# Performance work log

Hardware: AMD Instinct MI355X
Metric: run time of the kernel (lower is better)

Reference implementation:

```python
import jax, jax.numpy as jnp
import numpy as np

HEADS = 16
DIM_HEAD = 64
SCALE = DIM_HEAD ** -0.5
LN_EPS = 1e-5


def setup_inputs() -> dict:
    key = jax.random.key(0)
    ks = jax.random.split(key, 4)
    B, N, D = 2, 2048, 1024
    inner = HEADS * DIM_HEAD  # 1024
    x = jax.random.normal(ks[0], (B, N, D), dtype=jnp.float32)
    m = jax.random.normal(ks[1], (B, N, N), dtype=jnp.float32)
    gamma = jnp.ones((D,), dtype=jnp.float32)
    beta = jnp.zeros((D,), dtype=jnp.float32)
    W_qkv = jax.random.normal(ks[2], (D, 3 * inner), dtype=jnp.float32) * (D ** -0.5)
    W_out = jax.random.normal(ks[3], (inner, D), dtype=jnp.float32) * (inner ** -0.5)
    return {"x": x, "m": m, "gamma": gamma, "beta": beta, "W_qkv": W_qkv, "W_out": W_out}


def reference(x, m, gamma, beta, W_qkv, W_out):
    B, N, D = x.shape
    # LayerNorm
    mu = jnp.mean(x, axis=-1, keepdims=True)
    var = jnp.var(x, axis=-1, keepdims=True)
    xn = (x - mu) * jax.lax.rsqrt(var + LN_EPS) * gamma + beta
    # QKV projection (no bias)
    qkv = xn @ W_qkv  # [B, N, 3*inner]
    q, k, v = jnp.split(qkv, 3, axis=-1)
    split_heads = lambda t: t.reshape(B, N, HEADS, DIM_HEAD).transpose(0, 2, 1, 3)  # b h n d
    q, k, v = split_heads(q), split_heads(k), split_heads(v)
    # Non-standard order: mask added BEFORE scaling
    qk = jnp.einsum('bhid,bhjd->bhij', q, k)
    dots = (qk + m[:, None, :, :]) * SCALE
    attn = jax.nn.softmax(dots, axis=-1)
    out = jnp.einsum('bhij,bhjd->bhid', attn, v)
    out = out.transpose(0, 2, 1, 3).reshape(B, N, HEADS * DIM_HEAD)
    return out @ W_out  # dropout is identity at inference
```

## Files before the change

kernel.cpp:

```cpp
#include <hip/hip_runtime.h>
#include <hip/hip_bf16.h>
#include <math.h>

typedef _Float16 f16;
typedef _Float16 f16x4 __attribute__((ext_vector_type(4)));
typedef _Float16 f16x8 __attribute__((ext_vector_type(8)));
typedef float f32x4 __attribute__((ext_vector_type(4)));

#define HD 64
#define NH 16
#define BATCH 2
#define SEQ 2048
#define DMODEL 1024
#define NQKV 3072
#define ROWS 4096
#define NEG_BIG (-1.0e30f)
#define SCALE_LOG2E 0.18033688011112042f

__device__ __forceinline__ f32x4 mfma16h(f16x8 a, f16x8 b, f32x4 c){
  return __builtin_amdgcn_mfma_f32_16x16x32_f16(a, b, c, 0, 0, 0);
}

__device__ __forceinline__ void gload16(const f16* g, f16* l){
  __builtin_amdgcn_global_load_lds(
      (const __attribute__((address_space(1))) unsigned int*)(g),
      (__attribute__((address_space(3))) unsigned int*)(l), 16, 0, 0);
}

__global__ __launch_bounds__(256) void ln_kernel(const float* __restrict__ x,
    const float* __restrict__ gamma, const float* __restrict__ beta,
    f16* __restrict__ xn)
{
  int row = blockIdx.x;
  int tid = threadIdx.x;
  float4 v = ((const float4*)(x + (size_t)row * DMODEL))[tid];
  float s  = v.x + v.y + v.z + v.w;
  float s2 = v.x*v.x + v.y*v.y + v.z*v.z + v.w*v.w;
  #pragma unroll
  for (int off = 32; off; off >>= 1){ s += __shfl_xor(s, off); s2 += __shfl_xor(s2, off); }
  __shared__ float red[8];
  int wave = tid >> 6, lane = tid & 63;
  if (lane == 0){ red[wave] = s; red[4 + wave] = s2; }
  __syncthreads();
  s  = red[0] + red[1] + red[2] + red[3];
  s2 = red[4] + red[5] + red[6] + red[7];
  float mu  = s * (1.f / DMODEL);
  float var = s2 * (1.f / DMODEL) - mu * mu;
  float rs  = rsqrtf(var + 1e-5f);
  float4 g  = ((const float4*)gamma)[tid];
  float4 be = ((const float4*)beta)[tid];
  f16x4 o;
  o[0] = (f16)((v.x - mu) * rs * g.x + be.x);
  o[1] = (f16)((v.y - mu) * rs * g.y + be.y);
  o[2] = (f16)((v.z - mu) * rs * g.z + be.z);
  o[3] = (f16)((v.w - mu) * rs * g.w + be.w);
  *(f16x4*)(xn + (size_t)row * DMODEL + tid*4) = o;
}

__global__ __launch_bounds__(256) void transpose_f2h_kernel(const float* __restrict__ in,
    f16* __restrict__ out, int R, int C)
{
  __shared__ float t[32][33];
  int c0 = blockIdx.x * 32, r0 = blockIdx.y * 32;
  int lx = threadIdx.x & 31, ly = threadIdx.x >> 5;
  #pragma unroll
  for (int i = 0; i < 32; i += 8) t[ly + i][lx] = in[(size_t)(r0 + ly + i) * C + c0 + lx];
  __syncthreads();
  #pragma unroll
  for (int i = 0; i < 32; i += 8) out[(size_t)(c0 + ly + i) * R + r0 + lx] = (f16)t[lx][ly + i];
}


__global__ __launch_bounds__(256, 3) void gemm_qkv(const f16* __restrict__ A,
    const f16* __restrict__ Bt, f16* __restrict__ Qo, f16* __restrict__ Ko,
    f16* __restrict__ Vo)
{
  __shared__ __align__(16) f16 As[2][128][32];
  __shared__ __align__(16) f16 Bs[2][128][32];
  const int K = DMODEL;
  int bm = blockIdx.y * 128, bn = blockIdx.x * 128;
  int tid = threadIdx.x;
  int wave = tid >> 6, lane = tid & 63, quad = lane >> 4, l15 = lane & 15;
  int mw = (wave >> 1) * 64, nw = (wave & 1) * 64;

  int sr0 = wave*16 + (lane >> 2);
  int sr1 = sr0 + 64;
  int sc  = (lane & 3) ^ (sr0 & 3);
  const f16* Ag = A  + (size_t)bm * K;
  const f16* Bg = Bt + (size_t)bn * K;
  f16* ldsA0 = &As[0][wave*16     ][0];
  f16* ldsA1 = &As[0][wave*16 + 64][0];
  f16* ldsB0 = &Bs[0][wave*16     ][0];
  f16* ldsB1 = &Bs[0][wave*16 + 64][0];

#define QSTAGE(buf, k0) do{ \
    gload16(Ag + (size_t)sr0 * K + (k0) + sc*8, ldsA0 + (buf)*4096); \
    gload16(Ag + (size_t)sr1 * K + (k0) + sc*8, ldsA1 + (buf)*4096); \
    gload16(Bg + (size_t)sr0 * K + (k0) + sc*8, ldsB0 + (buf)*4096); \
    gload16(Bg + (size_t)sr1 * K + (k0) + sc*8, ldsB1 + (buf)*4096); }while(0)

  f32x4 zero = {0.f, 0.f, 0.f, 0.f};
  f32x4 acc[4][4];
  #pragma unroll
  for (int i = 0; i < 4; i++)
    #pragma unroll
    for (int j = 0; j < 4; j++) acc[i][j] = zero;

  QSTAGE(0, 0);
  const int NS = K / 32;
  for (int it = 0; it < NS; ++it){
    int cur = it & 1;
    asm volatile("s_waitcnt vmcnt(0)" ::: "memory");
    __syncthreads();
    if (it + 1 < NS) QSTAGE(cur ^ 1, (it + 1) * 32);
    int ca = (quad ^ (l15 & 3)) * 8;
    f16x8 af[4], bfr[4];
    #pragma unroll
    for (int i = 0; i < 4; i++) af[i]  = *(const f16x8*)&As[cur][mw + i*16 + l15][ca];
    #pragma unroll
    for (int i = 0; i < 4; i++) bfr[i] = *(const f16x8*)&Bs[cur][nw + i*16 + l15][ca];
    __builtin_amdgcn_s_setprio(1);
    #pragma unroll
    for (int mi = 0; mi < 4; mi++)
      #pragma unroll
      for (int ni = 0; ni < 4; ni++)
        acc[mi][ni] = mfma16h(af[mi], bfr[ni], acc[mi][ni]);
    __builtin_amdgcn_s_setprio(0);
  }
#undef QSTAGE

  #pragma unroll
  for (int mi = 0; mi < 4; mi++){
    #pragma unroll
    for (int ni = 0; ni < 4; ni++){
      #pragma unroll
      for (int reg = 0; reg < 4; reg++){
        int r = bm + mw + mi*16 + quad*4 + reg;
        int c = bn + nw + ni*16 + l15;
        float v = acc[mi][ni][reg];
        int which = c >> 10;
        int hc = c & 1023;
        int h = hc >> 6, d = hc & 63;
        int b = r >> 11, nseq = r & 2047;
        size_t bh = (size_t)(b * NH + h);
        if (which == 0)      Qo[(bh * SEQ + nseq) * HD + d] = (f16)v;
        else if (which == 1) Ko[(bh * SEQ + nseq) * HD + d] = (f16)v;
        else                 Vo[(bh * HD + d) * SEQ + nseq] = (f16)v;
      }
    }
  }
}

__global__ __launch_bounds__(256, 3) void gemm_out(const f16* __restrict__ A,
    const f16* __restrict__ Bt, float* __restrict__ C, int M, int N, int K)
{
  __shared__ __align__(16) f16 As[2][128][32];
  __shared__ __align__(16) f16 Bs[2][128][32];
  int bm = blockIdx.y * 128, bn = blockIdx.x * 128;
  int tid = threadIdx.x;
  int wave = tid >> 6, lane = tid & 63, quad = lane >> 4, l15 = lane & 15;
  int mw = (wave >> 1) * 64, nw = (wave & 1) * 64;

  int sr0 = wave*16 + (lane >> 2);
  int sr1 = sr0 + 64;
  int sc  = (lane & 3) ^ (sr0 & 3);
  const f16* Ag = A  + (size_t)bm * K;
  const f16* Bg = Bt + (size_t)bn * K;
  f16* ldsA0 = &As[0][wave*16     ][0];
  f16* ldsA1 = &As[0][wave*16 + 64][0];
  f16* ldsB0 = &Bs[0][wave*16     ][0];
  f16* ldsB1 = &Bs[0][wave*16 + 64][0];

#define OSTAGE(buf, k0) do{ \
    gload16(Ag + (size_t)sr0 * K + (k0) + sc*8, ldsA0 + (buf)*4096); \
    gload16(Ag + (size_t)sr1 * K + (k0) + sc*8, ldsA1 + (buf)*4096); \
    gload16(Bg + (size_t)sr0 * K + (k0) + sc*8, ldsB0 + (buf)*4096); \
    gload16(Bg + (size_t)sr1 * K + (k0) + sc*8, ldsB1 + (buf)*4096); }while(0)

  f32x4 zero = {0.f, 0.f, 0.f, 0.f};
  f32x4 acc[4][4];
  #pragma unroll
  for (int i = 0; i < 4; i++)
    #pragma unroll
    for (int j = 0; j < 4; j++) acc[i][j] = zero;

  OSTAGE(0, 0);
  const int NS = 1024 / 32;
  for (int it = 0; it < NS; ++it){
    int cur = it & 1;
    asm volatile("s_waitcnt vmcnt(0)" ::: "memory");
    __syncthreads();
    if (it + 1 < NS) OSTAGE(cur ^ 1, (it + 1) * 32);
    int ca = (quad ^ (l15 & 3)) * 8;
    f16x8 af[4], bfr[4];
    #pragma unroll
    for (int i = 0; i < 4; i++) af[i]  = *(const f16x8*)&As[cur][mw + i*16 + l15][ca];
    #pragma unroll
    for (int i = 0; i < 4; i++) bfr[i] = *(const f16x8*)&Bs[cur][nw + i*16 + l15][ca];
    __builtin_amdgcn_s_setprio(1);
    #pragma unroll
    for (int mi = 0; mi < 4; mi++)
      #pragma unroll
      for (int ni = 0; ni < 4; ni++)
        acc[mi][ni] = mfma16h(af[mi], bfr[ni], acc[mi][ni]);
    __builtin_amdgcn_s_setprio(0);
  }
#undef OSTAGE

  #pragma unroll
  for (int mi = 0; mi < 4; mi++)
    #pragma unroll
    for (int ni = 0; ni < 4; ni++)
      #pragma unroll
      for (int reg = 0; reg < 4; reg++){
        int r = bm + mw + mi*16 + quad*4 + reg;
        int c = bn + nw + ni*16 + l15;
        C[(size_t)r * N + c] = acc[mi][ni][reg];
      }
}

__global__ __launch_bounds__(256, 4) void attn_kernel(const f16* __restrict__ Q,
    const f16* __restrict__ Kb, const f16* __restrict__ Vt,
    const float* __restrict__ mask, f16* __restrict__ Ao)
{
  __shared__ __align__(16) f16 KsB[2][64*64];
  __shared__ __align__(16) f16 VsB[2][64*64];
  __shared__ __align__(16) f16 Ps[4*16*64];

  int bh = blockIdx.y; int b = bh >> 4; int h = bh & 15;
  int q0 = blockIdx.x * 64;
  int tid = threadIdx.x;
  int wave = tid >> 6, lane = tid & 63, quad = lane >> 4, l15 = lane & 15;

  int rA = (wave*2 + 0)*8 + (lane >> 3);
  int rB = (wave*2 + 1)*8 + (lane >> 3);
  int cp = lane & 7;
  int ccA = cp ^ (rA & 7);
  int ccB = cp ^ (rB & 7);
  const f16* Kg = Kb + (size_t)bh * SEQ * HD;
  const f16* Vg = Vt + (size_t)bh * HD * SEQ;
  f16* ldsKA = &KsB[0][0] + (wave*2 + 0)*8*64;
  f16* ldsKB = &KsB[0][0] + (wave*2 + 1)*8*64;
  f16* ldsVA = &VsB[0][0] + (wave*2 + 0)*8*64;
  f16* ldsVB = &VsB[0][0] + (wave*2 + 1)*8*64;

  f16x8 qf[2];
  {
    const f16* qrow = Q + ((size_t)bh * SEQ + q0 + wave*16 + l15) * HD + quad*8;
    qf[0] = *(const f16x8*)(qrow);
    qf[1] = *(const f16x8*)(qrow + 32);
  }

  const float* mrow = mask + ((size_t)b * SEQ + q0 + wave*16 + l15) * SEQ + quad*4;

  gload16(Kg + (size_t)(0 + rA)*HD + ccA*8, ldsKA);
  gload16(Kg + (size_t)(0 + rB)*HD + ccB*8, ldsKB);
  gload16(Vg + (size_t)rA*SEQ + 0 + ccA*8, ldsVA);
  gload16(Vg + (size_t)rB*SEQ + 0 + ccB*8, ldsVB);

  f32x4 zero = {0.f, 0.f, 0.f, 0.f};
  f32x4 O[4];
  #pragma unroll
  for (int nt = 0; nt < 4; nt++) O[nt] = zero;
  float mrun = NEG_BIG, lrun = 0.f;

  const int NT = SEQ / 64;
  for (int it = 0; it < NT; ++it){
    int cur = it & 1;
    int j0 = it * 64;
    asm volatile("s_waitcnt vmcnt(0)" ::: "memory");
    __syncthreads();
    if (it + 1 < NT){
      int nb = cur ^ 1;
      int j0n = j0 + 64;
      gload16(Kg + (size_t)(j0n + rA)*HD + ccA*8, ldsKA + nb*4096);
      gload16(Kg + (size_t)(j0n + rB)*HD + ccB*8, ldsKB + nb*4096);
      gload16(Vg + (size_t)rA*SEQ + j0n + ccA*8, ldsVA + nb*4096);
      gload16(Vg + (size_t)rB*SEQ + j0n + ccB*8, ldsVB + nb*4096);
    }
    const f16* Ksc = &KsB[cur][0];
    const f16* Vsc = &VsB[cur][0];

    float sv[4][4];
    __builtin_amdgcn_s_setprio(1);
    #pragma unroll
    for (int jt = 0; jt < 4; jt++){
      f32x4 a = zero;
      int r = jt*16 + l15;
      #pragma unroll
      for (int kk = 0; kk < 2; kk++){
        f16x8 kf = *(const f16x8*)&Ksc[r*64 + (((kk*4 + quad) ^ (r & 7))*8)];
        a = mfma16h(kf, qf[kk], a);
      }
      float4 mv = *(const float4*)(mrow + j0 + jt*16);
      sv[jt][0] = (a[0] + mv.x) * SCALE_LOG2E;
      sv[jt][1] = (a[1] + mv.y) * SCALE_LOG2E;
      sv[jt][2] = (a[2] + mv.z) * SCALE_LOG2E;
      sv[jt][3] = (a[3] + mv.w) * SCALE_LOG2E;
    }
    __builtin_amdgcn_s_setprio(0);

    float m0 = fmaxf(fmaxf(sv[0][0], sv[0][1]), fmaxf(sv[0][2], sv[0][3]));
    float m1 = fmaxf(fmaxf(sv[1][0], sv[1][1]), fmaxf(sv[1][2], sv[1][3]));
    float m2 = fmaxf(fmaxf(sv[2][0], sv[2][1]), fmaxf(sv[2][2], sv[2][3]));
    float m3 = fmaxf(fmaxf(sv[3][0], sv[3][1]), fmaxf(sv[3][2], sv[3][3]));
    float tmax = fmaxf(fmaxf(m0, m1), fmaxf(m2, m3));
    tmax = fmaxf(tmax, __shfl_xor(tmax, 16));
    tmax = fmaxf(tmax, __shfl_xor(tmax, 32));

    if (__any(tmax > mrun + 8.f)){
      float nm = fmaxf(mrun, tmax);
      float alpha = exp2f(mrun - nm);
      mrun = nm;
      lrun *= alpha;
      float aR[4];
      #pragma unroll
      for (int reg = 0; reg < 4; reg++)
        aR[reg] = __shfl(alpha, (lane & 48) | (quad*4 + reg));
      #pragma unroll
      for (int nt = 0; nt < 4; nt++)
        #pragma unroll
        for (int reg = 0; reg < 4; reg++) O[nt][reg] *= aR[reg];
    }

    float ps = 0.f;
    #pragma unroll
    for (int jt = 0; jt < 4; jt++)
      #pragma unroll
      for (int reg = 0; reg < 4; reg++){
        float p = exp2f(sv[jt][reg] - mrun);
        sv[jt][reg] = p; ps += p;
      }
    ps += __shfl_xor(ps, 16);
    ps += __shfl_xor(ps, 32);
    lrun += ps;

    #pragma unroll
    for (int jt = 0; jt < 4; jt++){
      f16x4 ph;
      ph[0] = (f16)sv[jt][0]; ph[1] = (f16)sv[jt][1];
      ph[2] = (f16)sv[jt][2]; ph[3] = (f16)sv[jt][3];
      *(f16x4*)&Ps[wave*1024 + l15*64 + (((jt*2 + (quad>>1)) ^ (l15 & 7))*8) + (quad & 1)*4] = ph;
    }

    __builtin_amdgcn_s_setprio(1);
    #pragma unroll
    for (int nt = 0; nt < 4; nt++){
      #pragma unroll
      for (int kk = 0; kk < 2; kk++){
        int rv = nt*16 + l15;
        f16x8 pf = *(const f16x8*)&Ps[wave*1024 + l15*64 + (((kk*4 + quad) ^ (l15 & 7))*8)];
        f16x8 vf = *(const f16x8*)&Vsc[rv*64 + (((kk*4 + quad) ^ (rv & 7))*8)];
        O[nt] = mfma16h(pf, vf, O[nt]);
      }
    }
    __builtin_amdgcn_s_setprio(0);
  }

  float lR[4];
  #pragma unroll
  for (int reg = 0; reg < 4; reg++)
    lR[reg] = __shfl(lrun, (lane & 48) | (quad*4 + reg));
  #pragma unroll
  for (int nt = 0; nt < 4; nt++){
    #pragma unroll
    for (int reg = 0; reg < 4; reg++){
      float o = O[nt][reg] / lR[reg];
      int r = q0 + wave*16 + quad*4 + reg;
      Ao[((size_t)(b * SEQ + r)) * DMODEL + h * HD + nt*16 + l15] = (f16)o;
    }
  }
}

extern "C" void kernel_launch(void* const* d_in, const int* in_sizes, int n_in,
                              void* d_out, int out_size, void* d_ws, size_t ws_size,
                              hipStream_t stream)
{
  (void)in_sizes; (void)n_in; (void)out_size; (void)ws_size;
  const float* x     = (const float*)d_in[0];
  const float* m     = (const float*)d_in[1];
  const float* gamma = (const float*)d_in[2];
  const float* beta  = (const float*)d_in[3];
  const float* Wqkv  = (const float*)d_in[4];
  const float* Wout  = (const float*)d_in[5];
  float* out = (float*)d_out;

  char* ws = (char*)d_ws;
  f16* xn    = (f16*)(ws + 0);
  f16* Ao    = (f16*)(ws + 0);
  f16* Qb    = (f16*)(ws + 8388608);
  f16* WoutT = (f16*)(ws + 8388608);
  f16* Kbuf  = (f16*)(ws + 16777216);
  f16* Vtb   = (f16*)(ws + 25165824);
  f16* WqkvT = (f16*)(ws + 33554432);

  ln_kernel<<<ROWS, 256, 0, stream>>>(x, gamma, beta, xn);
  transpose_f2h_kernel<<<dim3(NQKV/32, DMODEL/32), 256, 0, stream>>>(Wqkv, WqkvT, DMODEL, NQKV);
  gemm_qkv<<<dim3(NQKV/128, ROWS/128), 256, 0, stream>>>(xn, WqkvT, Qb, Kbuf, Vtb);
  attn_kernel<<<dim3(SEQ/64, BATCH*NH), 256, 0, stream>>>(Qb, Kbuf, Vtb, m, Ao);
  transpose_f2h_kernel<<<dim3(DMODEL/32, DMODEL/32), 256, 0, stream>>>(Wout, WoutT, DMODEL, DMODEL);
  gemm_out<<<dim3(DMODEL/128, ROWS/128), 256, 0, stream>>>(Ao, WoutT, out, ROWS, DMODEL, DMODEL);
}
```

Before: 270.2 us.

## Load K/V fragments directly into registers in attention, halve gemm_out M tile

The attention kernel no longer stages K and V through double-buffered LDS with barriers. Each wave loads its K and V MFMA fragments straight from global memory into registers, prefetching the next K tile during the softmax. The per-tile cross-lane row-sum shuffle is deferred to a single reduction after the loop. The output GEMM tile is reduced from 128x128 to 64x128 to launch more blocks, at the cost of redundant per-wave global loads of K/V (no sharing across waves) and higher register pressure.

Result: slower. 450.1 us (+66.6%).

```diff
diff --git a/kernel.cpp b/kernel.cpp
--- a/kernel.cpp
+++ b/kernel.cpp
@@ -70,7 +70,6 @@
   for (int i = 0; i < 32; i += 8) out[(size_t)(c0 + ly + i) * R + r0 + lx] = (f16)t[lx][ly + i];
 }
 
-
 __global__ __launch_bounds__(256, 3) void gemm_qkv(const f16* __restrict__ A,
     const f16* __restrict__ Bt, f16* __restrict__ Qo, f16* __restrict__ Ko,
     f16* __restrict__ Vo)
@@ -151,55 +150,52 @@
   }
 }
 
-__global__ __launch_bounds__(256, 3) void gemm_out(const f16* __restrict__ A,
+__global__ __launch_bounds__(256, 4) void gemm_out(const f16* __restrict__ A,
     const f16* __restrict__ Bt, float* __restrict__ C, int M, int N, int K)
 {
-  __shared__ __align__(16) f16 As[2][128][32];
+  __shared__ __align__(16) f16 As[2][64][32];
   __shared__ __align__(16) f16 Bs[2][128][32];
-  int bm = blockIdx.y * 128, bn = blockIdx.x * 128;
+  int bm = blockIdx.y * 64, bn = blockIdx.x * 128;
   int tid = threadIdx.x;
   int wave = tid >> 6, lane = tid & 63, quad = lane >> 4, l15 = lane & 15;
-  int mw = (wave >> 1) * 64, nw = (wave & 1) * 64;
+  int mw = (wave >> 1) * 32, nw = (wave & 1) * 64;
 
   int sr0 = wave*16 + (lane >> 2);
-  int sr1 = sr0 + 64;
   int sc  = (lane & 3) ^ (sr0 & 3);
   const f16* Ag = A  + (size_t)bm * K;
   const f16* Bg = Bt + (size_t)bn * K;
   f16* ldsA0 = &As[0][wave*16     ][0];
-  f16* ldsA1 = &As[0][wave*16 + 64][0];
   f16* ldsB0 = &Bs[0][wave*16     ][0];
   f16* ldsB1 = &Bs[0][wave*16 + 64][0];
 
 #define OSTAGE(buf, k0) do{ \
-    gload16(Ag + (size_t)sr0 * K + (k0) + sc*8, ldsA0 + (buf)*4096); \
-    gload16(Ag + (size_t)sr1 * K + (k0) + sc*8, ldsA1 + (buf)*4096); \
+    gload16(Ag + (size_t)sr0 * K + (k0) + sc*8, ldsA0 + (buf)*2048); \
     gload16(Bg + (size_t)sr0 * K + (k0) + sc*8, ldsB0 + (buf)*4096); \
-    gload16(Bg + (size_t)sr1 * K + (k0) + sc*8, ldsB1 + (buf)*4096); }while(0)
+    gload16(Bg + (size_t)(sr0 + 64) * K + (k0) + sc*8, ldsB1 + (buf)*4096); }while(0)
 
   f32x4 zero = {0.f, 0.f, 0.f, 0.f};
-  f32x4 acc[4][4];
-  #pragma unroll
-  for (int i = 0; i < 4; i++)
+  f32x4 acc[2][4];
+  #pragma unroll
+  for (int i = 0; i < 2; i++)
     #pragma unroll
     for (int j = 0; j < 4; j++) acc[i][j] = zero;
 
   OSTAGE(0, 0);
-  const int NS = 1024 / 32;
+  const int NS = DMODEL / 32;
   for (int it = 0; it < NS; ++it){
     int cur = it & 1;
     asm volatile("s_waitcnt vmcnt(0)" ::: "memory");
     __syncthreads();
     if (it + 1 < NS) OSTAGE(cur ^ 1, (it + 1) * 32);
     int ca = (quad ^ (l15 & 3)) * 8;
-    f16x8 af[4], bfr[4];
-    #pragma unroll
-    for (int i = 0; i < 4; i++) af[i]  = *(const f16x8*)&As[cur][mw + i*16 + l15][ca];
+    f16x8 af[2], bfr[4];
+    #pragma unroll
+    for (int i = 0; i < 2; i++) af[i]  = *(const f16x8*)&As[cur][mw + i*16 + l15][ca];
     #pragma unroll
     for (int i = 0; i < 4; i++) bfr[i] = *(const f16x8*)&Bs[cur][nw + i*16 + l15][ca];
     __builtin_amdgcn_s_setprio(1);
     #pragma unroll
-    for (int mi = 0; mi < 4; mi++)
+    for (int mi = 0; mi < 2; mi++)
       #pragma unroll
       for (int ni = 0; ni < 4; ni++)
         acc[mi][ni] = mfma16h(af[mi], bfr[ni], acc[mi][ni]);
@@ -208,7 +204,7 @@
 #undef OSTAGE
 
   #pragma unroll
-  for (int mi = 0; mi < 4; mi++)
+  for (int mi = 0; mi < 2; mi++)
     #pragma unroll
     for (int ni = 0; ni < 4; ni++)
       #pragma unroll
@@ -219,12 +215,10 @@
       }
 }
 
-__global__ __launch_bounds__(256, 4) void attn_kernel(const f16* __restrict__ Q,
+__global__ __launch_bounds__(256, 3) void attn_kernel(const f16* __restrict__ Q,
     const f16* __restrict__ Kb, const f16* __restrict__ Vt,
     const float* __restrict__ mask, f16* __restrict__ Ao)
 {
-  __shared__ __align__(16) f16 KsB[2][64*64];
-  __shared__ __align__(16) f16 VsB[2][64*64];
   __shared__ __align__(16) f16 Ps[4*16*64];
 
   int bh = blockIdx.y; int b = bh >> 4; int h = bh & 15;
@@ -232,17 +226,8 @@
   int tid = threadIdx.x;
   int wave = tid >> 6, lane = tid & 63, quad = lane >> 4, l15 = lane & 15;
 
-  int rA = (wave*2 + 0)*8 + (lane >> 3);
-  int rB = (wave*2 + 1)*8 + (lane >> 3);
-  int cp = lane & 7;
-  int ccA = cp ^ (rA & 7);
-  int ccB = cp ^ (rB & 7);
   const f16* Kg = Kb + (size_t)bh * SEQ * HD;
   const f16* Vg = Vt + (size_t)bh * HD * SEQ;
-  f16* ldsKA = &KsB[0][0] + (wave*2 + 0)*8*64;
-  f16* ldsKB = &KsB[0][0] + (wave*2 + 1)*8*64;
-  f16* ldsVA = &VsB[0][0] + (wave*2 + 0)*8*64;
-  f16* ldsVB = &VsB[0][0] + (wave*2 + 1)*8*64;
 
   f16x8 qf[2];
   {
@@ -253,52 +238,55 @@
 
   const float* mrow = mask + ((size_t)b * SEQ + q0 + wave*16 + l15) * SEQ + quad*4;
 
-  gload16(Kg + (size_t)(0 + rA)*HD + ccA*8, ldsKA);
-  gload16(Kg + (size_t)(0 + rB)*HD + ccB*8, ldsKB);
-  gload16(Vg + (size_t)rA*SEQ + 0 + ccA*8, ldsVA);
-  gload16(Vg + (size_t)rB*SEQ + 0 + ccB*8, ldsVB);
-
   f32x4 zero = {0.f, 0.f, 0.f, 0.f};
   f32x4 O[4];
   #pragma unroll
   for (int nt = 0; nt < 4; nt++) O[nt] = zero;
   float mrun = NEG_BIG, lrun = 0.f;
 
+  f16x8 kf[8];
+  #pragma unroll
+  for (int jt = 0; jt < 4; jt++)
+    #pragma unroll
+    for (int kk = 0; kk < 2; kk++)
+      kf[jt*2+kk] = *(const f16x8*)(Kg + (size_t)(jt*16 + l15)*HD + kk*32 + quad*8);
+
   const int NT = SEQ / 64;
+  #pragma unroll 1
   for (int it = 0; it < NT; ++it){
-    int cur = it & 1;
     int j0 = it * 64;
-    asm volatile("s_waitcnt vmcnt(0)" ::: "memory");
-    __syncthreads();
-    if (it + 1 < NT){
-      int nb = cur ^ 1;
-      int j0n = j0 + 64;
-      gload16(Kg + (size_t)(j0n + rA)*HD + ccA*8, ldsKA + nb*4096);
-      gload16(Kg + (size_t)(j0n + rB)*HD + ccB*8, ldsKB + nb*4096);
-      gload16(Vg + (size_t)rA*SEQ + j0n + ccA*8, ldsVA + nb*4096);
-      gload16(Vg + (size_t)rB*SEQ + j0n + ccB*8, ldsVB + nb*4096);
-    }
-    const f16* Ksc = &KsB[cur][0];
-    const f16* Vsc = &VsB[cur][0];
+    int jn = (j0 + 64) & (SEQ - 1);
+
+    f16x8 vf[8];
+    #pragma unroll
+    for (int nt = 0; nt < 4; nt++)
+      #pragma unroll
+      for (int kk = 0; kk < 2; kk++)
+        vf[nt*2+kk] = *(const f16x8*)(Vg + (size_t)(nt*16 + l15)*SEQ + j0 + kk*32 + quad*8);
+
+    float4 mv[4];
+    #pragma unroll
+    for (int jt = 0; jt < 4; jt++) mv[jt] = *(const float4*)(mrow + j0 + jt*16);
 
     float sv[4][4];
     __builtin_amdgcn_s_setprio(1);
     #pragma unroll
     for (int jt = 0; jt < 4; jt++){
       f32x4 a = zero;
-      int r = jt*16 + l15;
-      #pragma unroll
-      for (int kk = 0; kk < 2; kk++){
-        f16x8 kf = *(const f16x8*)&Ksc[r*64 + (((kk*4 + quad) ^ (r & 7))*8)];
-        a = mfma16h(kf, qf[kk], a);
-      }
-      float4 mv = *(const float4*)(mrow + j0 + jt*16);
-      sv[jt][0] = (a[0] + mv.x) * SCALE_LOG2E;
-      sv[jt][1] = (a[1] + mv.y) * SCALE_LOG2E;
-      sv[jt][2] = (a[2] + mv.z) * SCALE_LOG2E;
-      sv[jt][3] = (a[3] + mv.w) * SCALE_LOG2E;
+      a = mfma16h(kf[jt*2 + 0], qf[0], a);
+      a = mfma16h(kf[jt*2 + 1], qf[1], a);
+      sv[jt][0] = (a[0] + mv[jt].x) * SCALE_LOG2E;
+      sv[jt][1] = (a[1] + mv[jt].y) * SCALE_LOG2E;
+      sv[jt][2] = (a[2] + mv[jt].z) * SCALE_LOG2E;
+      sv[jt][3] = (a[3] + mv[jt].w) * SCALE_LOG2E;
     }
     __builtin_amdgcn_s_setprio(0);
+
+    #pragma unroll
+    for (int jt = 0; jt < 4; jt++)
+      #pragma unroll
+      for (int kk = 0; kk < 2; kk++)
+        kf[jt*2+kk] = *(const f16x8*)(Kg + (size_t)(jn + jt*16 + l15)*HD + kk*32 + quad*8);
 
     float m0 = fmaxf(fmaxf(sv[0][0], sv[0][1]), fmaxf(sv[0][2], sv[0][3]));
     float m1 = fmaxf(fmaxf(sv[1][0], sv[1][1]), fmaxf(sv[1][2], sv[1][3]));
@@ -331,8 +319,6 @@
         float p = exp2f(sv[jt][reg] - mrun);
         sv[jt][reg] = p; ps += p;
       }
-    ps += __shfl_xor(ps, 16);
-    ps += __shfl_xor(ps, 32);
     lrun += ps;
 
     #pragma unroll
@@ -342,21 +328,20 @@
       ph[2] = (f16)sv[jt][2]; ph[3] = (f16)sv[jt][3];
       *(f16x4*)&Ps[wave*1024 + l15*64 + (((jt*2 + (quad>>1)) ^ (l15 & 7))*8) + (quad & 1)*4] = ph;
     }
+    f16x8 pf0 = *(const f16x8*)&Ps[wave*1024 + l15*64 + (((0*4 + quad) ^ (l15 & 7))*8)];
+    f16x8 pf1 = *(const f16x8*)&Ps[wave*1024 + l15*64 + (((1*4 + quad) ^ (l15 & 7))*8)];
 
     __builtin_amdgcn_s_setprio(1);
     #pragma unroll
     for (int nt = 0; nt < 4; nt++){
-      #pragma unroll
-      for (int kk = 0; kk < 2; kk++){
-        int rv = nt*16 + l15;
-        f16x8 pf = *(const f16x8*)&Ps[wave*1024 + l15*64 + (((kk*4 + quad) ^ (l15 & 7))*8)];
-        f16x8 vf = *(const f16x8*)&Vsc[rv*64 + (((kk*4 + quad) ^ (rv & 7))*8)];
-        O[nt] = mfma16h(pf, vf, O[nt]);
-      }
+      O[nt] = mfma16h(pf0, vf[nt*2 + 0], O[nt]);
+      O[nt] = mfma16h(pf1, vf[nt*2 + 1], O[nt]);
     }
     __builtin_amdgcn_s_setprio(0);
   }
 
+  lrun += __shfl_xor(lrun, 16);
+  lrun += __shfl_xor(lrun, 32);
   float lR[4];
   #pragma unroll
   for (int reg = 0; reg < 4; reg++)
@@ -399,5 +384,5 @@
   gemm_qkv<<<dim3(NQKV/128, ROWS/128), 256, 0, stream>>>(xn, WqkvT, Qb, Kbuf, Vtb);
   attn_kernel<<<dim3(SEQ/64, BATCH*NH), 256, 0, stream>>>(Qb, Kbuf, Vtb, m, Ao);
   transpose_f2h_kernel<<<dim3(DMODEL/32, DMODEL/32), 256, 0, stream>>>(Wout, WoutT, DMODEL, DMODEL);
-  gemm_out<<<dim3(DMODEL/128, ROWS/128), 256, 0, stream>>>(Ao, WoutT, out, ROWS, DMODEL, DMODEL);
-}
+  gemm_out<<<dim3(DMODEL/128, ROWS/64), 256, 0, stream>>>(Ao, WoutT, out, ROWS, DMODEL, DMODEL);
+}
```
